# Optimization experiments

Measured on AMD Instinct MI355X. Metric: run time of the kernel, lower is better.

## Reference

```python
import jax, jax.numpy as jnp
import numpy as np

B, N, D_IMG = 64, 196, 2048
T = 32
V, E, H, A = 32000, 512, 1024, 256
PAD_ID = 0


def setup_inputs() -> dict:
    key = jax.random.key(0)
    ks = jax.random.split(key, 16)
    s = lambda *sh: 1.0 / np.sqrt(sh[-1])
    img_seq = jax.random.normal(ks[0], (B, N, D_IMG), dtype=jnp.float32)
    tokens_in = jax.random.randint(ks[1], (B, T), 0, V, dtype=jnp.int64)
    embed = jax.random.normal(ks[2], (V, E), dtype=jnp.float32) * 0.02
    embed = embed.at[PAD_ID].set(0.0)  # padding_idx row is zero
    W_head1 = jax.random.normal(ks[3], (E, E + D_IMG), dtype=jnp.float32) * s(E + D_IMG)
    W_ih = jax.random.normal(ks[4], (4 * H, E), dtype=jnp.float32) * s(H)
    W_hh = jax.random.normal(ks[5], (4 * H, H), dtype=jnp.float32) * s(H)
    b_ih = jax.random.normal(ks[6], (4 * H,), dtype=jnp.float32) * s(H)
    b_hh = jax.random.normal(ks[7], (4 * H,), dtype=jnp.float32) * s(H)
    W_head = jax.random.normal(ks[8], (V, H), dtype=jnp.float32) * s(H)
    W_img = jax.random.normal(ks[9], (A, D_IMG), dtype=jnp.float32) * s(D_IMG)
    W_hid = jax.random.normal(ks[10], (A, H), dtype=jnp.float32) * s(H)
    w_score = jax.random.normal(ks[11], (A,), dtype=jnp.float32) * s(A)
    W_h0 = jax.random.normal(ks[12], (H, D_IMG), dtype=jnp.float32) * s(D_IMG)
    b_h0 = jax.random.normal(ks[13], (H,), dtype=jnp.float32) * s(D_IMG)
    W_c0 = jax.random.normal(ks[14], (H, D_IMG), dtype=jnp.float32) * s(D_IMG)
    b_c0 = jax.random.normal(ks[15], (H,), dtype=jnp.float32) * s(D_IMG)
    return dict(img_seq=img_seq, tokens_in=tokens_in, embed=embed, W_head1=W_head1,
                W_ih=W_ih, W_hh=W_hh, b_ih=b_ih, b_hh=b_hh, W_head=W_head,
                W_img=W_img, W_hid=W_hid, w_score=w_score,
                W_h0=W_h0, b_h0=b_h0, W_c0=W_c0, b_c0=b_c0)


def _decode(img_seq, tokens_in, embed, W_head1, W_ih, W_hh, b_ih, b_hh,
            W_head, W_img, W_hid, w_score, W_h0, b_h0, W_c0, b_c0):
    g = img_seq.mean(axis=1)                              # [B, D]
    h = jnp.tanh(g @ W_h0.T + b_h0)                       # [B, H]
    c = jnp.tanh(g @ W_c0.T + b_c0)                       # [B, H]
    # image projection is time-invariant: hoist out of the loop
    proj_img = jnp.einsum('bnd,ad->bna', img_seq, W_img)  # [B, N, A]
    emb_all = embed[tokens_in]                            # [B, T, E]

    def step(carry, emb_t):
        h, c = carry
        # additive attention
        proj_h = h @ W_hid.T                              # [B, A]
        scores = jnp.einsum('bna,a->bn', jnp.tanh(proj_img + proj_h[:, None, :]), w_score)
        weights = jax.nn.softmax(scores, axis=-1)         # [B, N]
        ctx = jnp.einsum('bn,bnd->bd', weights, img_seq)  # [B, D]
        x = jnp.concatenate([emb_t, ctx], axis=-1) @ W_head1.T  # [B, E]
        # LSTMCell (PyTorch gate order: i, f, g, o)
        gates = x @ W_ih.T + b_ih + h @ W_hh.T + b_hh     # [B, 4H]
        i, f, gg, o = jnp.split(gates, 4, axis=-1)
        c_new = jax.nn.sigmoid(f) * c + jax.nn.sigmoid(i) * jnp.tanh(gg)
        h_new = jax.nn.sigmoid(o) * jnp.tanh(c_new)
        logits = h_new @ W_head.T                         # [B, V]
        return (h_new, c_new), logits

    _, ys = jax.lax.scan(step, (h, c), jnp.swapaxes(emb_all, 0, 1))  # ys: [T, B, V]
    return jnp.swapaxes(ys, 0, 1)                         # [B, T, V]


def reference(img_seq, tokens_in, embed, W_head1, W_ih, W_hh, b_ih, b_hh,
              W_head, W_img, W_hid, w_score, W_h0, b_h0, W_c0, b_c0):
    return _decode(img_seq, tokens_in, embed, W_head1, W_ih, W_hh, b_ih, b_hh,
                   W_head, W_img, W_hid, w_score, W_h0, b_h0, W_c0, b_c0)
```

## Files before the change

kernel.cpp:

```cpp
#include <hip/hip_runtime.h>
#include <stdint.h>

typedef unsigned short u16;
typedef __bf16 bf16x8 __attribute__((ext_vector_type(8)));
typedef float f32x4 __attribute__((ext_vector_type(4)));

#define DEV static __device__ __forceinline__

DEV u16 f2bu(float f) {
    union { float f; unsigned u; } v; v.f = f;
    unsigned r = v.u + 0x7FFFu + ((v.u >> 16) & 1u);
    return (u16)(r >> 16);
}
DEV float b2f(u16 b) {
    union { unsigned u; float f; } v; v.u = ((unsigned)b) << 16;
    return v.f;
}
DEV float fast_tanh(float x) {
    float e = __expf(2.f * x);
    return 1.f - __fdividef(2.f, e + 1.f);
}
DEV float fast_sig(float x) {
    return __fdividef(1.f, 1.f + __expf(-x));
}
DEV void gload_lds(const u16* g, u16* l) {
    __builtin_amdgcn_global_load_lds((const __attribute__((address_space(1))) void*)g,
                                     (__attribute__((address_space(3))) void*)l, 16, 0, 0);
}

template<bool A_F32, bool B_F32, bool B_KXN, bool OUT_BF16, bool BIAS>
__global__ __launch_bounds__(256) void gemm128(
    const void* __restrict__ Ap, int lda,
    const void* __restrict__ Bp, int ldb,
    void* __restrict__ Cp, int ldc,
    const float* __restrict__ bias, int K)
{
    __shared__ u16 As[128 * 40];
    __shared__ u16 Bs[128 * 40];
    const int tid = threadIdx.x;
    const int lane = tid & 63, wave = tid >> 6;
    const int wr = wave >> 1, wc = wave & 1;
    const int m0 = blockIdx.y * 128, n0 = blockIdx.x * 128;

    f32x4 acc[4][4];
#pragma unroll
    for (int m = 0; m < 4; ++m)
#pragma unroll
        for (int n = 0; n < 4; ++n)
            acc[m][n] = (f32x4){0.f, 0.f, 0.f, 0.f};

    for (int k0 = 0; k0 < K; k0 += 32) {
        __syncthreads();
        if (A_F32) {
            const float* A = (const float*)Ap;
#pragma unroll
            for (int i = 0; i < 4; ++i) {
                int c = tid + i * 256;
                int row = c >> 3, kc = (c & 7) * 4;
                float4 v = *(const float4*)&A[(size_t)(m0 + row) * lda + k0 + kc];
                ushort4 o; o.x = f2bu(v.x); o.y = f2bu(v.y); o.z = f2bu(v.z); o.w = f2bu(v.w);
                *(ushort4*)&As[row * 40 + kc] = o;
            }
        } else {
            const u16* A = (const u16*)Ap;
#pragma unroll
            for (int i = 0; i < 2; ++i) {
                int c = tid + i * 256;
                int row = c >> 2, kc = (c & 3) * 8;
                *(int4*)&As[row * 40 + kc] = *(const int4*)&A[(size_t)(m0 + row) * lda + k0 + kc];
            }
        }
        if (B_KXN) {
            const float* B = (const float*)Bp;
#pragma unroll
            for (int i = 0; i < 4; ++i) {
                int c = tid + i * 256;
                int kk = c >> 5, nc = (c & 31) * 4;
                float4 v = *(const float4*)&B[(size_t)(k0 + kk) * ldb + n0 + nc];
                Bs[(nc + 0) * 40 + kk] = f2bu(v.x);
                Bs[(nc + 1) * 40 + kk] = f2bu(v.y);
                Bs[(nc + 2) * 40 + kk] = f2bu(v.z);
                Bs[(nc + 3) * 40 + kk] = f2bu(v.w);
            }
        } else if (B_F32) {
            const float* B = (const float*)Bp;
#pragma unroll
            for (int i = 0; i < 4; ++i) {
                int c = tid + i * 256;
                int row = c >> 3, kc = (c & 7) * 4;
                float4 v = *(const float4*)&B[(size_t)(n0 + row) * ldb + k0 + kc];
                ushort4 o; o.x = f2bu(v.x); o.y = f2bu(v.y); o.z = f2bu(v.z); o.w = f2bu(v.w);
                *(ushort4*)&Bs[row * 40 + kc] = o;
            }
        } else {
            const u16* B = (const u16*)Bp;
#pragma unroll
            for (int i = 0; i < 2; ++i) {
                int c = tid + i * 256;
                int row = c >> 2, kc = (c & 3) * 8;
                *(int4*)&Bs[row * 40 + kc] = *(const int4*)&B[(size_t)(n0 + row) * ldb + k0 + kc];
            }
        }
        __syncthreads();
        const int fr = lane & 15, kq = (lane >> 4) * 8;
        bf16x8 af[4], bq[4];
#pragma unroll
        for (int m = 0; m < 4; ++m)
            af[m] = *(const bf16x8*)&As[(wr * 64 + m * 16 + fr) * 40 + kq];
#pragma unroll
        for (int n = 0; n < 4; ++n)
            bq[n] = *(const bf16x8*)&Bs[(wc * 64 + n * 16 + fr) * 40 + kq];
#pragma unroll
        for (int m = 0; m < 4; ++m)
#pragma unroll
            for (int n = 0; n < 4; ++n)
                acc[m][n] = __builtin_amdgcn_mfma_f32_16x16x32_bf16(af[m], bq[n], acc[m][n], 0, 0, 0);
    }
    const int fr = lane & 15, rq = (lane >> 4) * 4;
#pragma unroll
    for (int m = 0; m < 4; ++m) {
#pragma unroll
        for (int n = 0; n < 4; ++n) {
            int col = n0 + wc * 64 + n * 16 + fr;
            float bv = BIAS ? bias[col] : 0.f;
#pragma unroll
            for (int r = 0; r < 4; ++r) {
                int row = m0 + wr * 64 + m * 16 + rq + r;
                float v = acc[m][n][r] + bv;
                if (OUT_BF16) ((u16*)Cp)[(size_t)row * ldc + col] = f2bu(v);
                else          ((float*)Cp)[(size_t)row * ldc + col] = v;
            }
        }
    }
}

__global__ __launch_bounds__(256) void gemm_head(const u16* __restrict__ A,
                                                 const u16* __restrict__ B,
                                                 float* __restrict__ C)
{
    __shared__ u16 As[128 * 32];
    __shared__ u16 Bs[128 * 32];
    const int tid = threadIdx.x, lane = tid & 63, wave = tid >> 6;
    const int wr = wave >> 1, wc = wave & 1;
    int bid = blockIdx.x;
    int nb = (bid & 7) * 500 + (bid >> 3);
    const int m0 = (nb & 15) * 128;
    const int n0 = (nb >> 4) * 128;

    f32x4 acc[4][4];
#pragma unroll
    for (int m = 0; m < 4; ++m)
#pragma unroll
        for (int n = 0; n < 4; ++n)
            acc[m][n] = (f32x4){0.f, 0.f, 0.f, 0.f};

    const int srow = lane >> 2;
    const int sk = (lane & 3) * 8;
    const int fr = lane & 15, kq = (lane >> 4) * 8;

    for (int k0 = 0; k0 < 1024; k0 += 32) {
        __syncthreads();
#pragma unroll
        for (int j = 0; j < 2; ++j) {
            const int rb = (j * 4 + wave) * 16;
            gload_lds(&A[(size_t)(m0 + rb + srow) * 1024 + k0 + sk], &As[rb * 32]);
            gload_lds(&B[(size_t)(n0 + rb + srow) * 1024 + k0 + sk], &Bs[rb * 32]);
        }
        __syncthreads();
        bf16x8 af[4], bq[4];
#pragma unroll
        for (int m = 0; m < 4; ++m)
            af[m] = *(const bf16x8*)&As[(wr * 64 + m * 16 + fr) * 32 + kq];
#pragma unroll
        for (int n = 0; n < 4; ++n)
            bq[n] = *(const bf16x8*)&Bs[(wc * 64 + n * 16 + fr) * 32 + kq];
#pragma unroll
        for (int m = 0; m < 4; ++m)
#pragma unroll
            for (int n = 0; n < 4; ++n)
                acc[m][n] = __builtin_amdgcn_mfma_f32_16x16x32_bf16(af[m], bq[n], acc[m][n], 0, 0, 0);
    }
    const int rq = (lane >> 4) * 4;
#pragma unroll
    for (int m = 0; m < 4; ++m)
#pragma unroll
        for (int n = 0; n < 4; ++n) {
            int col = n0 + wc * 64 + n * 16 + fr;
#pragma unroll
            for (int r = 0; r < 4; ++r)
                C[(size_t)(m0 + wr * 64 + m * 16 + rq + r) * 32000 + col] = acc[m][n][r];
        }
}

__global__ __launch_bounds__(256) void prep_k(
    const float* __restrict__ img, const float* __restrict__ Whh,
    const float* __restrict__ Whid, const float* __restrict__ Whead,
    const int* __restrict__ tok, const float* __restrict__ embed,
    const float* __restrict__ bih, const float* __restrict__ bhh,
    u16* __restrict__ img_bf, u16* __restrict__ Whh_bf,
    u16* __restrict__ Whid_bf, u16* __restrict__ Whead_bf,
    u16* __restrict__ emb_bf, float* __restrict__ bsum)
{
    const int bid = blockIdx.x;
    if (bid < 25088) {
        int i = bid * 256 + threadIdx.x;
        float4 v = ((const float4*)img)[i];
        ushort4 o; o.x = f2bu(v.x); o.y = f2bu(v.y); o.z = f2bu(v.z); o.w = f2bu(v.w);
        ((ushort4*)img_bf)[i] = o;
    } else if (bid < 29184) {
        int i = (bid - 25088) * 256 + threadIdx.x;
        float4 v = ((const float4*)Whh)[i];
        ushort4 o; o.x = f2bu(v.x); o.y = f2bu(v.y); o.z = f2bu(v.z); o.w = f2bu(v.w);
        ((ushort4*)Whh_bf)[i] = o;
    } else if (bid < 29440) {
        int i = (bid - 29184) * 256 + threadIdx.x;
        float4 v = ((const float4*)Whid)[i];
        ushort4 o; o.x = f2bu(v.x); o.y = f2bu(v.y); o.z = f2bu(v.z); o.w = f2bu(v.w);
        ((ushort4*)Whid_bf)[i] = o;
    } else if (bid < 61440) {
        int i = (bid - 29440) * 256 + threadIdx.x;
        float4 v = ((const float4*)Whead)[i];
        ushort4 o; o.x = f2bu(v.x); o.y = f2bu(v.y); o.z = f2bu(v.z); o.w = f2bu(v.w);
        ((ushort4*)Whead_bf)[i] = o;
    } else if (bid < 65536) {
        int id = (bid - 61440) * 256 + threadIdx.x;
        int row = id >> 9, e = id & 511;
        int t = row >> 6, b = row & 63;
        int tk = tok[b * 32 + t];
        emb_bf[(size_t)row * 512 + e] = f2bu(embed[(size_t)tk * 512 + e]);
    } else {
        int i = (bid - 65536) * 256 + threadIdx.x;
        bsum[i] = bih[i] + bhh[i];
    }
}

__global__ __launch_bounds__(256) void pack_w(const u16* __restrict__ Wic,
                                              const u16* __restrict__ Whh,
                                              u16* __restrict__ Wpk)
{
    const int bid = blockIdx.y;
    const int t2 = blockIdx.x * 256 + threadIdx.x;
    const int i = t2 >> 6, lane = t2 & 63;
    const int fr = lane & 15, kq = (lane >> 4) * 8;
    const int grow = ((fr >> 2) << 10) + bid * 4 + (fr & 3);
    const int k0 = i * 32;
    int4 v;
    if (k0 < 2048) v = *(const int4*)&Wic[(size_t)grow * 2048 + k0 + kq];
    else           v = *(const int4*)&Whh[(size_t)grow * 1024 + (k0 - 2048) + kq];
    *(int4*)&Wpk[((size_t)bid * 6144 + t2) * 8] = v;
}

__global__ __launch_bounds__(256) void mean_k(const u16* __restrict__ img_bf, float* __restrict__ gT)
{
    int id = blockIdx.x * 256 + threadIdx.x;
    int b = id >> 10;
    int d = (id & 1023) * 2;
    const u16* base = img_bf + (size_t)b * 196 * 2048 + d;
    float s0 = 0.f, s1 = 0.f;
#pragma unroll 4
    for (int n = 0; n < 196; ++n) {
        ushort2 v = *(const ushort2*)(base + (size_t)n * 2048);
        s0 += b2f(v.x);
        s1 += b2f(v.y);
    }
    gT[(d + 0) * 64 + b] = s0 * (1.f / 196.f);
    gT[(d + 1) * 64 + b] = s1 * (1.f / 196.f);
}

__global__ __launch_bounds__(256) void h0c0(const float* __restrict__ gT,
                                            const float* __restrict__ Wh0, const float* __restrict__ bh0,
                                            const float* __restrict__ Wc0, const float* __restrict__ bc0,
                                            float* __restrict__ c, u16* __restrict__ h0)
{
    int id = blockIdx.x * 256 + threadIdx.x;
    int b = id & 63, n = id >> 6;
    const float4* Wh = (const float4*)&Wh0[(size_t)n * 2048];
    const float4* Wc = (const float4*)&Wc0[(size_t)n * 2048];
    float s0 = 0.f, s1 = 0.f;
#pragma unroll 4
    for (int k4 = 0; k4 < 512; ++k4) {
        float4 wh = Wh[k4], wc = Wc[k4];
        float g0 = gT[(k4 * 4 + 0) * 64 + b];
        float g1 = gT[(k4 * 4 + 1) * 64 + b];
        float g2 = gT[(k4 * 4 + 2) * 64 + b];
        float g3 = gT[(k4 * 4 + 3) * 64 + b];
        s0 += wh.x * g0 + wh.y * g1 + wh.z * g2 + wh.w * g3;
        s1 += wc.x * g0 + wc.y * g1 + wc.z * g2 + wc.w * g3;
    }
    c[b * 1024 + n] = fast_tanh(s1 + bc0[n]);
    h0[(size_t)b * 1024 + n] = f2bu(fast_tanh(s0 + bh0[n]));
}


__global__ __launch_bounds__(512) void ph_k(const u16* __restrict__ hb,
                                            const u16* __restrict__ Whid_bf,
                                            float* __restrict__ ph_all)
{
    const int tid = threadIdx.x, lane = tid & 63, wave = tid >> 6;
    const int fr = lane & 15, kq = (lane >> 4) * 8, rq = (lane >> 4) * 4;
    const int a0 = blockIdx.x * 16;
    __shared__ float red[8][64][16];
    f32x4 acc[4];
#pragma unroll
    for (int m = 0; m < 4; ++m) acc[m] = (f32x4){0.f, 0.f, 0.f, 0.f};
#pragma unroll
    for (int kk = 0; kk < 128; kk += 32) {
        const int k0 = wave * 128 + kk;
        bf16x8 bq = *(const bf16x8*)&Whid_bf[(size_t)(a0 + fr) * 1024 + k0 + kq];
#pragma unroll
        for (int m = 0; m < 4; ++m) {
            bf16x8 af = *(const bf16x8*)&hb[(size_t)(m * 16 + fr) * 1024 + k0 + kq];
            acc[m] = __builtin_amdgcn_mfma_f32_16x16x32_bf16(af, bq, acc[m], 0, 0, 0);
        }
    }
#pragma unroll
    for (int m = 0; m < 4; ++m)
#pragma unroll
        for (int r = 0; r < 4; ++r)
            red[wave][m * 16 + rq + r][fr] = acc[m][r];
    __syncthreads();
#pragma unroll
    for (int i = 0; i < 2; ++i) {
        const int idx = tid + i * 512;
        const int bb = idx >> 4, a = idx & 15;
        float s = 0.f;
#pragma unroll
        for (int w8 = 0; w8 < 8; ++w8) s += red[w8][bb][a];
        ph_all[bb * 256 + a0 + a] = s;
    }
}

__global__ __launch_bounds__(512) void attn_k(const float* __restrict__ ph_all,
                                              const float* __restrict__ w_score,
                                              const u16* __restrict__ proj_bf,
                                              const u16* __restrict__ img_bf,
                                              u16* __restrict__ ctx_bf)
{
    const int b = blockIdx.x >> 2, q = blockIdx.x & 3;
    const int tid = threadIdx.x, lane = tid & 63, wave = tid >> 6;
    __shared__ float ph[256], ws[256], sc[256], red[256];
    __shared__ float part[8][512];
    if (tid < 256) {
        ph[tid] = ph_all[b * 256 + tid];
        ws[tid] = w_score[tid];
        sc[tid] = -1e30f;
    }
    __syncthreads();
    for (int n = wave; n < 196; n += 8) {
        const int a0 = lane * 4;
        ushort4 pv = *(const ushort4*)&proj_bf[((size_t)b * 196 + n) * 256 + a0];
        float s = ws[a0 + 0] * fast_tanh(b2f(pv.x) + ph[a0 + 0])
                + ws[a0 + 1] * fast_tanh(b2f(pv.y) + ph[a0 + 1])
                + ws[a0 + 2] * fast_tanh(b2f(pv.z) + ph[a0 + 2])
                + ws[a0 + 3] * fast_tanh(b2f(pv.w) + ph[a0 + 3]);
#pragma unroll
        for (int off = 32; off; off >>= 1) s += __shfl_xor(s, off, 64);
        if (lane == 0) sc[n] = s;
    }
    __syncthreads();
    if (tid < 256) red[tid] = sc[tid];
    __syncthreads();
#pragma unroll
    for (int s2 = 128; s2 > 0; s2 >>= 1) {
        if (tid < s2) red[tid] = fmaxf(red[tid], red[tid + s2]);
        __syncthreads();
    }
    const float mx = red[0];
    __syncthreads();
    float e = (tid < 196) ? __expf(sc[tid] - mx) : 0.f;
    if (tid < 256) red[tid] = e;
    __syncthreads();
#pragma unroll
    for (int s2 = 128; s2 > 0; s2 >>= 1) {
        if (tid < s2) red[tid] += red[tid + s2];
        __syncthreads();
    }
    const float inv = __fdividef(1.f, red[0]);
    __syncthreads();
    if (tid < 256) sc[tid] = e * inv;
    __syncthreads();
    const int gid = tid >> 3, st = tid & 7;
    const int c0 = q * 512 + gid * 8;
    const u16* base = img_bf + ((size_t)b * 196) * 2048 + c0;
    float a[8];
#pragma unroll
    for (int i = 0; i < 8; ++i) a[i] = 0.f;
    for (int n = st; n < 196; n += 8) {
        bf16x8 v = *(const bf16x8*)(base + (size_t)n * 2048);
        float wgt = sc[n];
#pragma unroll
        for (int i = 0; i < 8; ++i) a[i] += wgt * (float)v[i];
    }
#pragma unroll
    for (int i = 0; i < 8; ++i) part[st][gid * 8 + i] = a[i];
    __syncthreads();
    const int col = tid;
    float v = part[0][col] + part[1][col] + part[2][col] + part[3][col]
            + part[4][col] + part[5][col] + part[6][col] + part[7][col];
    ctx_bf[(size_t)b * 2048 + q * 512 + col] = f2bu(v);
}

__global__ __launch_bounds__(512) void gates_k(const u16* __restrict__ ctx_bf,
                                               const u16* __restrict__ hb,
                                               const u16* __restrict__ Wpk,
                                               const float* __restrict__ xg,
                                               float* __restrict__ cbuf,
                                               u16* __restrict__ h_nxt,
                                               u16* __restrict__ h_all,
                                               int t)
{
    const int tid = threadIdx.x, lane = tid & 63, wave = tid >> 6;
    const int fr = lane & 15, kq = (lane >> 4) * 8, rq = (lane >> 4) * 4;
    const int hc0 = blockIdx.x * 4;
    const u16* Wblk = Wpk + (size_t)blockIdx.x * 49152 + lane * 8;
    __shared__ float red[8][64][16];

    f32x4 acc[4];
#pragma unroll
    for (int m = 0; m < 4; ++m) acc[m] = (f32x4){0.f, 0.f, 0.f, 0.f};

    const int kbeg = wave * 384, kend = kbeg + 384;
    const int cend = kend < 2048 ? kend : 2048;
#pragma unroll 4
    for (int k0 = kbeg; k0 < cend; k0 += 32) {
        bf16x8 bq = *(const bf16x8*)&Wblk[(size_t)(k0 >> 5) * 512];
#pragma unroll
        for (int m = 0; m < 4; ++m) {
            bf16x8 af = *(const bf16x8*)&ctx_bf[(size_t)(m * 16 + fr) * 2048 + k0 + kq];
            acc[m] = __builtin_amdgcn_mfma_f32_16x16x32_bf16(af, bq, acc[m], 0, 0, 0);
        }
    }
    const int hbeg = kbeg > 2048 ? kbeg - 2048 : 0;
    const int hend = kend > 2048 ? kend - 2048 : 0;
#pragma unroll 4
    for (int kh = hbeg; kh < hend; kh += 32) {
        bf16x8 bq = *(const bf16x8*)&Wblk[(size_t)((kh + 2048) >> 5) * 512];
#pragma unroll
        for (int m = 0; m < 4; ++m) {
            bf16x8 af = *(const bf16x8*)&hb[(size_t)(m * 16 + fr) * 1024 + kh + kq];
            acc[m] = __builtin_amdgcn_mfma_f32_16x16x32_bf16(af, bq, acc[m], 0, 0, 0);
        }
    }
#pragma unroll
    for (int m = 0; m < 4; ++m)
#pragma unroll
        for (int r = 0; r < 4; ++r)
            red[wave][m * 16 + rq + r][fr] = acc[m][r];
    __syncthreads();

    if (tid < 256) {
        const int bb = tid >> 2, j = tid & 3;
        const int col = hc0 + j;
        float G[4];
#pragma unroll
        for (int g = 0; g < 4; ++g) {
            const int f2 = g * 4 + j;
            float s = 0.f;
#pragma unroll
            for (int w8 = 0; w8 < 8; ++w8) s += red[w8][bb][f2];
            G[g] = s + xg[((size_t)t * 64 + bb) * 4096 + g * 1024 + col];
        }
        float ig = fast_sig(G[0]), fg = fast_sig(G[1]);
        float gv = fast_tanh(G[2]), og = fast_sig(G[3]);
        float cp = cbuf[bb * 1024 + col];
        float cn = fg * cp + ig * gv;
        cbuf[bb * 1024 + col] = cn;
        u16 hv = f2bu(og * fast_tanh(cn));
        h_nxt[(size_t)bb * 1024 + col] = hv;
        h_all[((size_t)bb * 32 + t) * 1024 + col] = hv;
    }
}

extern "C" void kernel_launch(void* const* d_in, const int* in_sizes, int n_in,
                              void* d_out, int out_size, void* d_ws, size_t ws_size,
                              hipStream_t stream)
{
    const float* img     = (const float*)d_in[0];
    const int*   tok     = (const int*)d_in[1];
    const float* embed   = (const float*)d_in[2];
    const float* W_head1 = (const float*)d_in[3];
    const float* W_ih    = (const float*)d_in[4];
    const float* W_hh    = (const float*)d_in[5];
    const float* b_ih    = (const float*)d_in[6];
    const float* b_hh    = (const float*)d_in[7];
    const float* W_head  = (const float*)d_in[8];
    const float* W_img   = (const float*)d_in[9];
    const float* W_hid   = (const float*)d_in[10];
    const float* w_score = (const float*)d_in[11];
    const float* W_h0    = (const float*)d_in[12];
    const float* b_h0    = (const float*)d_in[13];
    const float* W_c0    = (const float*)d_in[14];
    const float* b_c0    = (const float*)d_in[15];
    float* out = (float*)d_out;

    char* w = (char*)d_ws;
    size_t off = 0;
    auto alloc = [&](size_t bytes) { char* p = w + off; off += (bytes + 255) & ~(size_t)255; return p; };

    u16*   Wic      = (u16*)alloc(4096ULL * 2048 * 2);
    u16*   Whh_bf   = (u16*)alloc(4096ULL * 1024 * 2);
    u16*   Wpk      = (u16*)alloc(256ULL * 96 * 64 * 8 * 2);
    u16*   Whid_bf  = (u16*)alloc(256ULL * 1024 * 2);
    u16*   Whead_bf = (u16*)alloc(32000ULL * 1024 * 2);
    u16*   img_bf   = (u16*)alloc(64ULL * 196 * 2048 * 2);
    float* xg       = (float*)alloc(2048ULL * 4096 * 4);
    u16*   proj_bf  = (u16*)alloc(64ULL * 196 * 256 * 2);
    u16*   emb_bf   = (u16*)alloc(2048ULL * 512 * 2);
    u16*   xe       = (u16*)alloc(2048ULL * 512 * 2);
    float* gT       = (float*)alloc(2048ULL * 64 * 4);
    float* cbuf     = (float*)alloc(64ULL * 1024 * 4);
    u16*   hbuf     = (u16*)alloc(2ULL * 64 * 1024 * 2);
    u16*   ctx_bf   = (u16*)alloc(64ULL * 2048 * 2);
    u16*   h_all    = (u16*)alloc(2048ULL * 1024 * 2);
    float* ph_all   = (float*)alloc(64ULL * 256 * 4);
    float* bsum     = (float*)alloc(4096ULL * 4);
    (void)ws_size; (void)in_sizes; (void)n_in; (void)out_size;

    prep_k<<<dim3(65552), dim3(256), 0, stream>>>(img, W_hh, W_hid, W_head, tok, embed,
                                                  b_ih, b_hh, img_bf, Whh_bf, Whid_bf,
                                                  Whead_bf, emb_bf, bsum);
    mean_k<<<dim3(256), dim3(256), 0, stream>>>(img_bf, gT);
    h0c0<<<dim3(256), dim3(256), 0, stream>>>(gT, W_h0, b_h0, W_c0, b_c0, cbuf, hbuf);

    gemm128<false, true, false, true, false><<<dim3(4, 16), dim3(256), 0, stream>>>(
        emb_bf, 512, W_head1, 2560, xe, 512, nullptr, 512);
    gemm128<false, true, false, false, true><<<dim3(32, 16), dim3(256), 0, stream>>>(
        xe, 512, W_ih, 512, xg, 4096, bsum, 512);
    gemm128<true, true, true, true, false><<<dim3(16, 32), dim3(256), 0, stream>>>(
        W_ih, 512, W_head1 + 512, 2560, Wic, 2048, nullptr, 512);
    gemm128<false, true, false, true, false><<<dim3(2, 98), dim3(256), 0, stream>>>(
        img_bf, 2048, W_img, 2048, proj_bf, 256, nullptr, 2048);
    pack_w<<<dim3(24, 256), dim3(256), 0, stream>>>(Wic, Whh_bf, Wpk);

    for (int t = 0; t < 32; ++t) {
        u16* hb = hbuf + (size_t)(t & 1) * 65536;
        u16* hn = hbuf + (size_t)((t + 1) & 1) * 65536;
        ph_k<<<dim3(16), dim3(512), 0, stream>>>(hb, Whid_bf, ph_all);
        attn_k<<<dim3(256), dim3(512), 0, stream>>>(ph_all, w_score, proj_bf, img_bf, ctx_bf);
        gates_k<<<dim3(256), dim3(512), 0, stream>>>(ctx_bf, hb, Wpk, xg, cbuf, hn, h_all, t);
    }

    gemm_head<<<dim3(4000), dim3(256), 0, stream>>>(h_all, Whead_bf, out);
}
```

Before: 2.292 ms.

## Deepen head GEMM K-tile with XOR-swizzled LDS and double per-step kernel block size

The vocabulary-head GEMM now stages 64-wide K tiles instead of 32, with an XOR swizzle on LDS rows. This halves the number of barrier/load iterations and is meant to avoid LDS bank conflicts on the fragment reads. The per-timestep attention and gate kernels go from 512 to 1024 threads, splitting the N and K reductions over 16 waves instead of 8 to expose more parallelism in these latency-bound steps. The cost is larger shared-memory reduction buffers, more reduction work, and possible occupancy limits.

```diff
diff --git a/kernel.cpp b/kernel.cpp
--- a/kernel.cpp
+++ b/kernel.cpp
@@ -138,8 +138,8 @@
                                                  const u16* __restrict__ B,
                                                  float* __restrict__ C)
 {
-    __shared__ u16 As[128 * 32];
-    __shared__ u16 Bs[128 * 32];
+    __shared__ u16 As[128 * 64];
+    __shared__ u16 Bs[128 * 64];
     const int tid = threadIdx.x, lane = tid & 63, wave = tid >> 6;
     const int wr = wave >> 1, wc = wave & 1;
     int bid = blockIdx.x;
@@ -154,33 +154,43 @@
         for (int n = 0; n < 4; ++n)
             acc[m][n] = (f32x4){0.f, 0.f, 0.f, 0.f};
 
-    const int srow = lane >> 2;
-    const int sk = (lane & 3) * 8;
-    const int fr = lane & 15, kq = (lane >> 4) * 8;
-
-    for (int k0 = 0; k0 < 1024; k0 += 32) {
+    const int srg = lane >> 3;
+    const int sslot = lane & 7;
+    const int fr = lane & 15, kg = lane >> 4;
+
+    for (int k0 = 0; k0 < 1024; k0 += 64) {
         __syncthreads();
 #pragma unroll
-        for (int j = 0; j < 2; ++j) {
-            const int rb = (j * 4 + wave) * 16;
-            gload_lds(&A[(size_t)(m0 + rb + srow) * 1024 + k0 + sk], &As[rb * 32]);
-            gload_lds(&B[(size_t)(n0 + rb + srow) * 1024 + k0 + sk], &Bs[rb * 32]);
+        for (int j = 0; j < 4; ++j) {
+            const int rb = (j * 4 + wave) * 8;
+            const int ra = rb + srg;
+            const int ge = (sslot ^ (ra & 7)) * 8;
+            gload_lds(&A[(size_t)(m0 + ra) * 1024 + k0 + ge], &As[rb * 64]);
+            gload_lds(&B[(size_t)(n0 + ra) * 1024 + k0 + ge], &Bs[rb * 64]);
         }
         __syncthreads();
-        bf16x8 af[4], bq[4];
-#pragma unroll
-        for (int m = 0; m < 4; ++m)
-            af[m] = *(const bf16x8*)&As[(wr * 64 + m * 16 + fr) * 32 + kq];
-#pragma unroll
-        for (int n = 0; n < 4; ++n)
-            bq[n] = *(const bf16x8*)&Bs[(wc * 64 + n * 16 + fr) * 32 + kq];
-#pragma unroll
-        for (int m = 0; m < 4; ++m)
-#pragma unroll
-            for (int n = 0; n < 4; ++n)
-                acc[m][n] = __builtin_amdgcn_mfma_f32_16x16x32_bf16(af[m], bq[n], acc[m][n], 0, 0, 0);
-    }
-    const int rq = (lane >> 4) * 4;
+#pragma unroll
+        for (int kk = 0; kk < 2; ++kk) {
+            const int sl = kk * 4 + kg;
+            bf16x8 af[4], bq[4];
+#pragma unroll
+            for (int m = 0; m < 4; ++m) {
+                const int row = wr * 64 + m * 16 + fr;
+                af[m] = *(const bf16x8*)&As[row * 64 + ((sl ^ (row & 7)) << 3)];
+            }
+#pragma unroll
+            for (int n = 0; n < 4; ++n) {
+                const int row = wc * 64 + n * 16 + fr;
+                bq[n] = *(const bf16x8*)&Bs[row * 64 + ((sl ^ (row & 7)) << 3)];
+            }
+#pragma unroll
+            for (int m = 0; m < 4; ++m)
+#pragma unroll
+                for (int n = 0; n < 4; ++n)
+                    acc[m][n] = __builtin_amdgcn_mfma_f32_16x16x32_bf16(af[m], bq[n], acc[m][n], 0, 0, 0);
+        }
+    }
+    const int rq = kg * 4;
 #pragma unroll
     for (int m = 0; m < 4; ++m)
 #pragma unroll
@@ -330,23 +340,23 @@
     }
 }
 
-__global__ __launch_bounds__(512) void attn_k(const float* __restrict__ ph_all,
-                                              const float* __restrict__ w_score,
-                                              const u16* __restrict__ proj_bf,
-                                              const u16* __restrict__ img_bf,
-                                              u16* __restrict__ ctx_bf)
+__global__ __launch_bounds__(1024) void attn_k(const float* __restrict__ ph_all,
+                                               const float* __restrict__ w_score,
+                                               const u16* __restrict__ proj_bf,
+                                               const u16* __restrict__ img_bf,
+                                               u16* __restrict__ ctx_bf)
 {
     const int b = blockIdx.x >> 2, q = blockIdx.x & 3;
     const int tid = threadIdx.x, lane = tid & 63, wave = tid >> 6;
     __shared__ float ph[256], ws[256], sc[256], red[256];
-    __shared__ float part[8][512];
+    __shared__ float part[16][512];
     if (tid < 256) {
         ph[tid] = ph_all[b * 256 + tid];
         ws[tid] = w_score[tid];
         sc[tid] = -1e30f;
     }
     __syncthreads();
-    for (int n = wave; n < 196; n += 8) {
+    for (int n = wave; n < 196; n += 16) {
         const int a0 = lane * 4;
         ushort4 pv = *(const ushort4*)&proj_bf[((size_t)b * 196 + n) * 256 + a0];
         float s = ws[a0 + 0] * fast_tanh(b2f(pv.x) + ph[a0 + 0])
@@ -379,13 +389,13 @@
     __syncthreads();
     if (tid < 256) sc[tid] = e * inv;
     __syncthreads();
-    const int gid = tid >> 3, st = tid & 7;
+    const int gid = tid >> 4, st = tid & 15;
     const int c0 = q * 512 + gid * 8;
     const u16* base = img_bf + ((size_t)b * 196) * 2048 + c0;
     float a[8];
 #pragma unroll
     for (int i = 0; i < 8; ++i) a[i] = 0.f;
-    for (int n = st; n < 196; n += 8) {
+    for (int n = st; n < 196; n += 16) {
         bf16x8 v = *(const bf16x8*)(base + (size_t)n * 2048);
         float wgt = sc[n];
 #pragma unroll
@@ -394,34 +404,37 @@
 #pragma unroll
     for (int i = 0; i < 8; ++i) part[st][gid * 8 + i] = a[i];
     __syncthreads();
-    const int col = tid;
-    float v = part[0][col] + part[1][col] + part[2][col] + part[3][col]
-            + part[4][col] + part[5][col] + part[6][col] + part[7][col];
-    ctx_bf[(size_t)b * 2048 + q * 512 + col] = f2bu(v);
-}
-
-__global__ __launch_bounds__(512) void gates_k(const u16* __restrict__ ctx_bf,
-                                               const u16* __restrict__ hb,
-                                               const u16* __restrict__ Wpk,
-                                               const float* __restrict__ xg,
-                                               float* __restrict__ cbuf,
-                                               u16* __restrict__ h_nxt,
-                                               u16* __restrict__ h_all,
-                                               int t)
+    if (tid < 512) {
+        const int col = tid;
+        float v = 0.f;
+#pragma unroll
+        for (int s16 = 0; s16 < 16; ++s16) v += part[s16][col];
+        ctx_bf[(size_t)b * 2048 + q * 512 + col] = f2bu(v);
+    }
+}
+
+__global__ __launch_bounds__(1024) void gates_k(const u16* __restrict__ ctx_bf,
+                                                const u16* __restrict__ hb,
+                                                const u16* __restrict__ Wpk,
+                                                const float* __restrict__ xg,
+                                                float* __restrict__ cbuf,
+                                                u16* __restrict__ h_nxt,
+                                                u16* __restrict__ h_all,
+                                                int t)
 {
     const int tid = threadIdx.x, lane = tid & 63, wave = tid >> 6;
     const int fr = lane & 15, kq = (lane >> 4) * 8, rq = (lane >> 4) * 4;
     const int hc0 = blockIdx.x * 4;
     const u16* Wblk = Wpk + (size_t)blockIdx.x * 49152 + lane * 8;
-    __shared__ float red[8][64][16];
+    __shared__ float red[16][64][16];
 
     f32x4 acc[4];
 #pragma unroll
     for (int m = 0; m < 4; ++m) acc[m] = (f32x4){0.f, 0.f, 0.f, 0.f};
 
-    const int kbeg = wave * 384, kend = kbeg + 384;
+    const int kbeg = wave * 192, kend = kbeg + 192;
     const int cend = kend < 2048 ? kend : 2048;
-#pragma unroll 4
+#pragma unroll 2
     for (int k0 = kbeg; k0 < cend; k0 += 32) {
         bf16x8 bq = *(const bf16x8*)&Wblk[(size_t)(k0 >> 5) * 512];
 #pragma unroll
@@ -432,7 +445,7 @@
     }
     const int hbeg = kbeg > 2048 ? kbeg - 2048 : 0;
     const int hend = kend > 2048 ? kend - 2048 : 0;
-#pragma unroll 4
+#pragma unroll 2
     for (int kh = hbeg; kh < hend; kh += 32) {
         bf16x8 bq = *(const bf16x8*)&Wblk[(size_t)((kh + 2048) >> 5) * 512];
 #pragma unroll
@@ -457,7 +470,7 @@
             const int f2 = g * 4 + j;
             float s = 0.f;
 #pragma unroll
-            for (int w8 = 0; w8 < 8; ++w8) s += red[w8][bb][f2];
+            for (int w16 = 0; w16 < 16; ++w16) s += red[w16][bb][f2];
             G[g] = s + xg[((size_t)t * 64 + bb) * 4096 + g * 1024 + col];
         }
         float ig = fast_sig(G[0]), fg = fast_sig(G[1]);
@@ -536,8 +549,8 @@
         u16* hb = hbuf + (size_t)(t & 1) * 65536;
         u16* hn = hbuf + (size_t)((t + 1) & 1) * 65536;
         ph_k<<<dim3(16), dim3(512), 0, stream>>>(hb, Whid_bf, ph_all);
-        attn_k<<<dim3(256), dim3(512), 0, stream>>>(ph_all, w_score, proj_bf, img_bf, ctx_bf);
-        gates_k<<<dim3(256), dim3(512), 0, stream>>>(ctx_bf, hb, Wpk, xg, cbuf, hn, h_all, t);
+        attn_k<<<dim3(256), dim3(1024), 0, stream>>>(ph_all, w_score, proj_bf, img_bf, ctx_bf);
+        gates_k<<<dim3(256), dim3(1024), 0, stream>>>(ctx_bf, hb, Wpk, xg, cbuf, hn, h_all, t);
     }
 
     gemm_head<<<dim3(4000), dim3(256), 0, stream>>>(h_all, Whead_bf, out);
```

Result: faster. 2.023 ms (-11.7%).
